# Kernel optimization log

Measured on AMD Instinct MI355X. Metric: run time of the kernel, lower is better.

Reference implementation:

```python
import jax, jax.numpy as jnp
import numpy as np

K, S, PAD = 3, 2, 1
C, HID = 16, 128
H, W = 256, 256
EPS = 1e-6


def _unfold(xp, k, s):
    # xp: (B, C, Hp, Wp) -> (B, C*k*k, L), torch.nn.Unfold ordering (c major, then kh, kw)
    B, Cc, Hp, Wp = xp.shape
    Ho = (Hp - k) // s + 1
    Wo = (Wp - k) // s + 1
    cols = jnp.stack(
        [xp[:, :, i:i + (Ho - 1) * s + 1:s, j:j + (Wo - 1) * s + 1:s]
         for i in range(k) for j in range(k)], axis=2)  # (B, C, k*k, Ho, Wo)
    return cols.reshape(B, Cc * k * k, Ho * Wo), Ho, Wo


def _fold(patches, Hp, Wp, Ho, Wo, k, s):
    # patches: (B, C*k*k, L) -> scatter-add into (B, C, Hp, Wp)
    B = patches.shape[0]
    p = patches.reshape(B, -1, k, k, Ho, Wo)
    out = jnp.zeros((B, p.shape[1], Hp, Wp), dtype=patches.dtype)
    for i in range(k):
        for j in range(k):
            out = out.at[:, :, i:i + (Ho - 1) * s + 1:s, j:j + (Wo - 1) * s + 1:s].add(p[:, :, i, j])
    return out


def setup_inputs() -> dict:
    key = jax.random.key(0)
    ks = jax.random.split(key, 7)
    P = C * K * K  # 144
    x = jax.random.normal(ks[0], (32, C, H, W), dtype=jnp.float32)
    W1 = jax.random.normal(ks[1], (P, HID), dtype=jnp.float32) * (1.0 / np.sqrt(P))
    b1 = jax.random.normal(ks[2], (HID,), dtype=jnp.float32) * 0.01
    W2 = jax.random.normal(ks[3], (HID, P), dtype=jnp.float32) * (1.0 / np.sqrt(HID))
    b2 = jax.random.normal(ks[4], (P,), dtype=jnp.float32) * 0.01
    Wc = jax.random.normal(ks[5], (C, C), dtype=jnp.float32) * (1.0 / np.sqrt(C))
    bc = jax.random.normal(ks[6], (C,), dtype=jnp.float32) * 0.01
    return {"x": x, "W1": W1, "b1": b1, "W2": W2, "b2": b2, "Wc": Wc, "bc": bc}


def reference(x, W1, b1, W2, b2, Wc, bc):
    Hp, Wp = H + 2 * PAD, W + 2 * PAD
    xp = jnp.pad(x, ((0, 0), (0, 0), (PAD, PAD), (PAD, PAD)), mode='reflect')
    patches, Ho, Wo = _unfold(xp, K, S)          # (B, P, L)
    t = patches.transpose(0, 2, 1)               # (B, L, P)
    hcat = jax.nn.relu(t @ W1 + b1)              # (B, L, HID)
    out_p = (hcat @ W2 + b2).transpose(0, 2, 1)  # (B, P, L)
    folded = _fold(out_p, Hp, Wp, Ho, Wo, K, S)
    counts = _fold(jnp.ones_like(out_p), Hp, Wp, Ho, Wo, K, S)
    normalized = folded / (counts + EPS)
    logits = jnp.einsum('oc,bchw->bohw', Wc, normalized) + bc[None, :, None, None]
    attn = jax.nn.softmax(logits, axis=1)        # Softmax2d = softmax over channels
    modulated = normalized * attn
    return modulated[:, :, PAD:PAD + H, PAD:PAD + W]
```

## Files before the change

kernel.cpp:

```cpp
#include <hip/hip_runtime.h>
#include <math.h>

#define CC   16
#define HH   256
#define WW   256
#define HIDN 128
#define PDIM 144
#define K1PAD 160
#define PITCH_H 136

typedef _Float16 half8 __attribute__((ext_vector_type(8)));
typedef float   f32x4 __attribute__((ext_vector_type(4)));

#define MFMA16(a, b, c) __builtin_amdgcn_mfma_f32_16x16x32_f16((a), (b), (c), 0, 0, 0)

#define O_BYTES   ((size_t)524288 * 144 * 2)
#define W1T_OFF   O_BYTES
#define W1T_BYTES ((size_t)128 * K1PAD * 2)
#define W2T_OFF   (W1T_OFF + W1T_BYTES)
#define W2T_BYTES ((size_t)144 * 128 * 2)
#define WS_NEEDED (W2T_OFF + W2T_BYTES)

__device__ __forceinline__ void load_lds16(const float* g, float* l)
{
#if __has_builtin(__builtin_amdgcn_global_load_lds)
    __builtin_amdgcn_global_load_lds(
        (const __attribute__((address_space(1))) unsigned int*)g,
        (__attribute__((address_space(3))) unsigned int*)l, 16, 0, 0);
#else
    *(float4*)l = *(const float4*)g;
#endif
}

__device__ __forceinline__ void load_lds16h(const _Float16* g, _Float16* l)
{
#if __has_builtin(__builtin_amdgcn_global_load_lds)
    __builtin_amdgcn_global_load_lds(
        (const __attribute__((address_space(1))) unsigned int*)g,
        (__attribute__((address_space(3))) unsigned int*)l, 16, 0, 0);
#else
    *(float4*)(void*)l = *(const float4*)(const void*)g;
#endif
}

__global__ __launch_bounds__(256) void prep_kernel(
    const float* __restrict__ W1, const float* __restrict__ W2,
    _Float16* __restrict__ W1T, _Float16* __restrict__ W2T)
{
    const int idx = blockIdx.x * 256 + threadIdx.x;
    if (idx < 128 * K1PAD) {
        const int n = idx / K1PAD;
        const int k = idx - n * K1PAD;
        const int tap = k >> 4;
        const int c   = k & 15;
        W1T[idx] = (tap < 9) ? (_Float16)W1[(c * 9 + tap) * HIDN + n] : (_Float16)0.f;
    }
    if (idx < 144 * 128) {
        const int nn = idx >> 7;
        const int k  = idx & 127;
        const int tap = nn >> 4;
        const int c   = nn & 15;
        W2T[nn * 128 + k] = (_Float16)W2[k * PDIM + (c * 9 + tap)];
    }
}

__global__ __launch_bounds__(256) void mlp_kernel(
    const float* __restrict__ x,
    const _Float16* __restrict__ W1T, const float* __restrict__ b1,
    const _Float16* __restrict__ W2T, const float* __restrict__ b2,
    _Float16* __restrict__ og)
{
    __shared__ __align__(16) char smem[73728];
    _Float16* xT    = (_Float16*)smem;
    float*    xrowF = (float*)(smem + 24576);
    _Float16* hT    = (_Float16*)(smem + 24576);

    const int tid   = threadIdx.x;
    const int a     = blockIdx.x & 127;
    const int batch = blockIdx.x >> 7;
    const float* xb = x + (size_t)batch * CC * HH * WW;

    #pragma unroll
    for (int it = 0; it < 12; ++it) {
        const int idx = tid + it * 256;
        const int i   = idx >> 10;
        const int c   = (idx >> 6) & 15;
        const int q   = idx & 63;
        int ym = 2 * a + i - 1;
        if (ym < 0) ym = 1;
        load_lds16(xb + ((c * HH + ym) * WW + 4 * q), xrowF + idx * 4);
    }
    __syncthreads();

    #pragma unroll
    for (int k = 0; k < 3; ++k) {
        const int u  = tid + k * 256;
        const int i  = u >> 8;
        const int xm = u & 255;
        const float* rbase = xrowF + i * 4096 + xm;
        half8 lo, hi;
        #pragma unroll
        for (int c = 0; c < 8; ++c) lo[c] = (_Float16)rbase[c * 256];
        #pragma unroll
        for (int c = 0; c < 8; ++c) hi[c] = (_Float16)rbase[(c + 8) * 256];
        int s = u << 4;
        s ^= (s & 0x1C0) >> 3;
        *(half8*)(xT + s)       = lo;
        *(half8*)(xT + (s ^ 8)) = hi;
    }
    __syncthreads();

    const int wid  = tid >> 6;
    const int lane = tid & 63;
    const int l15  = lane & 15;
    const int quad = lane >> 4;
    const int qh   = quad >> 1;
    const int c0   = (quad & 1) * 8;

    {
        half8 bfr0[5], bfr1[5];
        float bias0, bias1;
        {
            const int nt0 = 2 * wid, nt1 = 2 * wid + 1;
            const _Float16* w0 = W1T + (nt0 * 16 + l15) * K1PAD + quad * 8;
            const _Float16* w1 = W1T + (nt1 * 16 + l15) * K1PAD + quad * 8;
            #pragma unroll
            for (int ks = 0; ks < 5; ++ks) {
                bfr0[ks] = *(const half8*)(w0 + ks * 32);
                bfr1[ks] = *(const half8*)(w1 + ks * 32);
            }
            bias0 = b1[nt0 * 16 + l15];
            bias1 = b1[nt1 * 16 + l15];
        }
        int koffU[5], koffF[5];
        #pragma unroll
        for (int ks = 0; ks < 5; ++ks) {
            int tap = 2 * ks + qh;
            if (tap > 8) tap = 8;
            const int i   = (tap * 11) >> 5;
            const int j   = tap - 3 * i;
            const int xmU = 2 * l15 + j - 1;
            const int xmF = (xmU < 0) ? 1 : xmU;
            koffU[ks] = (i << 12) + (xmU << 4) + c0;
            koffF[ks] = (i << 12) + (xmF << 4) + c0;
        }

        #define G1_STEP(MT, KO)                                                   \
        {                                                                         \
            f32x4 acc0 = {0.f, 0.f, 0.f, 0.f};                                    \
            f32x4 acc1 = {0.f, 0.f, 0.f, 0.f};                                    \
            _Pragma("unroll")                                                     \
            for (int ks = 0; ks < 5; ++ks) {                                      \
                int ix = KO[ks] + ((MT) << 9);                                    \
                ix ^= (ix & 0x1C0) >> 3;                                          \
                const half8 af = *(const half8*)(xT + ix);                        \
                acc0 = MFMA16(af, bfr0[ks], acc0);                                \
                acc1 = MFMA16(af, bfr1[ks], acc1);                                \
            }                                                                     \
            _Pragma("unroll")                                                     \
            for (int r = 0; r < 4; ++r) {                                         \
                const int row = (MT) * 16 + quad * 4 + r;                         \
                float h0 = acc0[r] + bias0;                                       \
                float h1 = acc1[r] + bias1;                                       \
                hT[row * PITCH_H + (2 * wid) * 16 + l15]     = (_Float16)(h0 > 0.f ? h0 : 0.f); \
                hT[row * PITCH_H + (2 * wid + 1) * 16 + l15] = (_Float16)(h1 > 0.f ? h1 : 0.f); \
            }                                                                     \
        }

        G1_STEP(0, koffF)
        for (int mt = 1; mt < 8; ++mt) G1_STEP(mt, koffU)
        #undef G1_STEP
    }
    __syncthreads();

    const size_t abase = ((size_t)batch * 128 + a) * 9;
    {
        half8 bfr2[2][4];
        float bias2[2];
        #pragma unroll
        for (int n = 0; n < 2; ++n) {
            const int nt = wid + n * 4;
            const _Float16* w2row = W2T + (nt * 16 + l15) * 128 + quad * 8;
            #pragma unroll
            for (int ks = 0; ks < 4; ++ks)
                bfr2[n][ks] = *(const half8*)(w2row + ks * 32);
            bias2[n] = b2[l15 * 9 + nt];
        }
        _Float16* ognA = og + (abase + wid) * 2048;
        _Float16* ognB = og + (abase + wid + 4) * 2048;
        for (int mt = 0; mt < 8; ++mt) {
            f32x4 acc0 = {0.f, 0.f, 0.f, 0.f};
            f32x4 acc1 = {0.f, 0.f, 0.f, 0.f};
            const _Float16* arow = hT + (mt * 16 + l15) * PITCH_H + quad * 8;
            #pragma unroll
            for (int ks = 0; ks < 4; ++ks) {
                const half8 af = *(const half8*)(arow + ks * 32);
                acc0 = MFMA16(af, bfr2[0][ks], acc0);
                acc1 = MFMA16(af, bfr2[1][ks], acc1);
            }
            #pragma unroll
            for (int r = 0; r < 4; ++r) {
                const int b = mt * 16 + quad * 4 + r;
                ognA[b * 16 + l15] = (_Float16)(acc0[r] + bias2[0]);
                ognB[b * 16 + l15] = (_Float16)(acc1[r] + bias2[1]);
            }
        }
        {
            half8 bfr8[4];
            const _Float16* w2row = W2T + (8 * 16 + l15) * 128 + quad * 8;
            #pragma unroll
            for (int ks = 0; ks < 4; ++ks)
                bfr8[ks] = *(const half8*)(w2row + ks * 32);
            const float bias8 = b2[l15 * 9 + 8];
            _Float16* ogn = og + (abase + 8) * 2048;
            #pragma unroll
            for (int m = 0; m < 2; ++m) {
                const int mt = 2 * wid + m;
                f32x4 acc = {0.f, 0.f, 0.f, 0.f};
                const _Float16* arow = hT + (mt * 16 + l15) * PITCH_H + quad * 8;
                #pragma unroll
                for (int ks = 0; ks < 4; ++ks)
                    acc = MFMA16(*(const half8*)(arow + ks * 32), bfr8[ks], acc);
                #pragma unroll
                for (int r = 0; r < 4; ++r) {
                    const int b = mt * 16 + quad * 4 + r;
                    ogn[b * 16 + l15] = (_Float16)(acc[r] + bias8);
                }
            }
        }
    }
}

__global__ __launch_bounds__(256) void gather_kernel(
    const _Float16* __restrict__ og, const float* __restrict__ Wc,
    const float* __restrict__ bc, float* __restrict__ out)
{
    __shared__ __align__(16) _Float16 sPl[9 * 2048];
    __shared__ float sWc[256];
    __shared__ float sbc[16];

    const int tid   = threadIdx.x;
    const int a     = blockIdx.x & 127;
    const int batch = blockIdx.x >> 7;

    sWc[tid] = Wc[tid];
    if (tid < 16) sbc[tid] = bc[tid];

    const size_t pb = (size_t)batch * 128;
    const int a1 = (a < 127) ? a + 1 : 127;
    const int srcOff = (tid ^ ((tid >> 3) & 7)) * 8;
    #pragma unroll
    for (int p = 0; p < 9; ++p) {
        const int ap  = (p < 6) ? a : a1;
        const int tap = (p < 3) ? (3 + p) : ((p < 6) ? (3 + p) : (p - 6));
        const _Float16* src = og + ((pb + ap) * 9 + tap) * 2048 + srcOff;
        load_lds16h(src, sPl + p * 2048 + tid * 8);
    }
    __syncthreads();

    const int x = tid;
    int blist[2], jlist[2], nb = 0;
    if ((x + 1) & 1) { blist[0] = x >> 1; jlist[0] = 1; nb = 1; }
    else {
        if (x < 255) { blist[nb] = (x + 1) >> 1; jlist[nb] = 0; ++nb; }
        blist[nb] = (x - 1) >> 1; jlist[nb] = 2; ++nb;
    }
    const int na1 = (a < 127) ? 2 : 1;

    float nrm0[CC], nrm1[CC];
    #pragma unroll
    for (int c = 0; c < CC; ++c) { nrm0[c] = 0.f; nrm1[c] = 0.f; }

    #define ACC_PLANE(P, B, DST)                                             \
    {                                                                        \
        int s = (B) * 16;                                                    \
        s ^= (s & 0x1C0) >> 3;                                               \
        const _Float16* orow = sPl + (P) * 2048;                             \
        const half8 o0 = *(const half8*)(orow + s);                          \
        const half8 o1 = *(const half8*)(orow + (s ^ 8));                    \
        _Pragma("unroll")                                                    \
        for (int e = 0; e < 8; ++e) { DST[e] += (float)o0[e]; DST[8 + e] += (float)o1[e]; } \
    }

    for (int v = 0; v < 2; ++v) {
        if (v >= nb) break;
        const int j = jlist[v];
        const int b = blist[v];
        ACC_PLANE(j,     b, nrm0)
        ACC_PLANE(3 + j, b, nrm1)
        if (na1 == 2) ACC_PLANE(6 + j, b, nrm1)
    }
    #undef ACC_PLANE

    const float inv0 = 1.f / ((float)nb + 1e-6f);
    const float inv1 = 1.f / ((float)(na1 * nb) + 1e-6f);
    #pragma unroll
    for (int c = 0; c < CC; ++c) { nrm0[c] *= inv0; nrm1[c] *= inv1; }

    const size_t obase = ((size_t)batch * CC) * (HH * WW) + (size_t)(2 * a) * WW + x;
    #pragma unroll
    for (int rowsel = 0; rowsel < 2; ++rowsel) {
        const float* nrm = rowsel ? nrm1 : nrm0;
        float lg[CC];
        #pragma unroll
        for (int o = 0; o < CC; ++o) {
            float s = sbc[o];
            #pragma unroll
            for (int c = 0; c < CC; ++c) s = fmaf(sWc[o * CC + c], nrm[c], s);
            lg[o] = s;
        }
        float mx = lg[0];
        #pragma unroll
        for (int o = 1; o < CC; ++o) mx = fmaxf(mx, lg[o]);
        float se = 0.f;
        #pragma unroll
        for (int o = 0; o < CC; ++o) { lg[o] = expf(lg[o] - mx); se += lg[o]; }
        const float isum = 1.f / se;
        const size_t ob = obase + (size_t)rowsel * WW;
        #pragma unroll
        for (int c = 0; c < CC; ++c)
            out[ob + (size_t)c * (HH * WW)] = nrm[c] * lg[c] * isum;
    }
}

#define HT_PITCH 68
__global__ __launch_bounds__(256) void mlp_fold_kernel_fb(
    const float* __restrict__ x,  const float* __restrict__ W1,
    const float* __restrict__ b1, const float* __restrict__ W2,
    const float* __restrict__ b2, float* __restrict__ folded)
{
    __shared__ __align__(16) float pT[PDIM * 64];
    __shared__ __align__(16) float hT[HIDN * HT_PITCH];
    const int tid = threadIdx.x;
    const int tile = blockIdx.x & 255;
    const int b = blockIdx.x >> 8;
    const int tile_base = tile * 64;
    const float* xb = x + (size_t)b * CC * HH * WW;
    for (int idx = tid; idx < PDIM * 64; idx += 256) {
        const int p = idx >> 6, lo = idx & 63;
        const int c = p / 9, rem = p - c * 9, i = rem / 3, j = rem - i * 3;
        const int l = tile_base + lo, a = l >> 7, bb = l & 127;
        int ym = 2 * a + i - 1, xm = 2 * bb + j - 1;
        if (ym < 0) ym = 1;
        if (xm < 0) xm = 1;
        pT[p * 64 + lo] = xb[(c * HH + ym) * WW + xm];
    }
    __syncthreads();
    {
        const int cg = tid & 31, rg = tid >> 5, rbase = rg * 8;
        float acc[8][4];
        #pragma unroll
        for (int m = 0; m < 8; ++m)
            #pragma unroll
            for (int jj = 0; jj < 4; ++jj) acc[m][jj] = 0.f;
        for (int k = 0; k < PDIM; ++k) {
            const float4 w = *reinterpret_cast<const float4*>(W1 + k * HIDN + cg * 4);
            const float4 pa = *reinterpret_cast<const float4*>(pT + k * 64 + rbase);
            const float4 pb2 = *reinterpret_cast<const float4*>(pT + k * 64 + rbase + 4);
            const float pv[8] = {pa.x, pa.y, pa.z, pa.w, pb2.x, pb2.y, pb2.z, pb2.w};
            const float wv[4] = {w.x, w.y, w.z, w.w};
            #pragma unroll
            for (int m = 0; m < 8; ++m)
                #pragma unroll
                for (int jj = 0; jj < 4; ++jj) acc[m][jj] = fmaf(pv[m], wv[jj], acc[m][jj]);
        }
        #pragma unroll
        for (int jj = 0; jj < 4; ++jj) {
            const int jcol = cg * 4 + jj;
            const float bj = b1[jcol];
            #pragma unroll
            for (int m = 0; m < 8; ++m) {
                const float hval = acc[m][jj] + bj;
                hT[jcol * HT_PITCH + rbase + m] = hval > 0.f ? hval : 0.f;
            }
        }
    }
    __syncthreads();
    {
        const int cg2 = tid & 15, rg2 = tid >> 4, rb2 = rg2 * 4;
        float acc2[4][9];
        #pragma unroll
        for (int m = 0; m < 4; ++m)
            #pragma unroll
            for (int jj = 0; jj < 9; ++jj) acc2[m][jj] = 0.f;
        const float* w2base = W2 + cg2 * 9;
        for (int h = 0; h < HIDN; ++h) {
            const float4 hv4 = *reinterpret_cast<const float4*>(hT + h * HT_PITCH + rb2);
            const float hv[4] = {hv4.x, hv4.y, hv4.z, hv4.w};
            float wv[9];
            #pragma unroll
            for (int jj = 0; jj < 9; ++jj) wv[jj] = w2base[h * PDIM + jj];
            #pragma unroll
            for (int m = 0; m < 4; ++m)
                #pragma unroll
                for (int jj = 0; jj < 9; ++jj) acc2[m][jj] = fmaf(hv[m], wv[jj], acc2[m][jj]);
        }
        float bv[9];
        #pragma unroll
        for (int jj = 0; jj < 9; ++jj) bv[jj] = b2[cg2 * 9 + jj];
        float* fb = folded + ((size_t)b * CC + cg2) * (HH * WW);
        #pragma unroll
        for (int m = 0; m < 4; ++m) {
            const int l = tile_base + rb2 + m, a = l >> 7, bb = l & 127;
            #pragma unroll
            for (int jj = 0; jj < 9; ++jj) {
                const int i = jj / 3, j2 = jj - i * 3;
                const int ypad = 2 * a + i, xpad = 2 * bb + j2;
                if (ypad >= 1 && xpad >= 1)
                    atomicAdd(fb + (ypad - 1) * WW + (xpad - 1), acc2[m][jj] + bv[jj]);
            }
        }
    }
}

__global__ __launch_bounds__(256) void norm_softmax_kernel_fb(
    float* __restrict__ out, const float* __restrict__ Wc, const float* __restrict__ bc)
{
    const int xo = threadIdx.x, yo = blockIdx.x & 255, b = blockIdx.x >> 8;
    const int yp = yo + 1, xp = xo + 1;
    const float cy = ((yp & 1) || yp == 256) ? 1.f : 2.f;
    const float cx = ((xp & 1) || xp == 256) ? 1.f : 2.f;
    const float inv = 1.f / (cy * cx + 1e-6f);
    const size_t base = ((size_t)b * CC) * (HH * WW) + (size_t)yo * WW + xo;
    float nrm[CC];
    #pragma unroll
    for (int c = 0; c < CC; ++c) nrm[c] = out[base + (size_t)c * (HH * WW)] * inv;
    float logits[CC];
    #pragma unroll
    for (int o = 0; o < CC; ++o) {
        float s = bc[o];
        #pragma unroll
        for (int c = 0; c < CC; ++c) s = fmaf(Wc[o * CC + c], nrm[c], s);
        logits[o] = s;
    }
    float mx = logits[0];
    #pragma unroll
    for (int o = 1; o < CC; ++o) mx = fmaxf(mx, logits[o]);
    float se = 0.f;
    #pragma unroll
    for (int o = 0; o < CC; ++o) { logits[o] = expf(logits[o] - mx); se += logits[o]; }
    const float isum = 1.f / se;
    #pragma unroll
    for (int c = 0; c < CC; ++c)
        out[base + (size_t)c * (HH * WW)] = nrm[c] * logits[c] * isum;
}

extern "C" void kernel_launch(void* const* d_in, const int* in_sizes, int n_in,
                              void* d_out, int out_size, void* d_ws, size_t ws_size,
                              hipStream_t stream)
{
    const float* x  = (const float*)d_in[0];
    const float* W1 = (const float*)d_in[1];
    const float* b1 = (const float*)d_in[2];
    const float* W2 = (const float*)d_in[3];
    const float* b2 = (const float*)d_in[4];
    const float* Wc = (const float*)d_in[5];
    const float* bc = (const float*)d_in[6];
    float* out = (float*)d_out;

    if (ws_size >= WS_NEEDED) {
        _Float16* og  = (_Float16*)d_ws;
        _Float16* W1T = (_Float16*)((char*)d_ws + W1T_OFF);
        _Float16* W2T = (_Float16*)((char*)d_ws + W2T_OFF);

        prep_kernel<<<dim3(80), dim3(256), 0, stream>>>(W1, W2, W1T, W2T);
        mlp_kernel<<<dim3(32 * 128), dim3(256), 0, stream>>>(x, W1T, b1, W2T, b2, og);
        gather_kernel<<<dim3(32 * 128), dim3(256), 0, stream>>>(og, Wc, bc, out);
    } else {
        hipMemsetAsync(d_out, 0, (size_t)out_size * sizeof(float), stream);
        mlp_fold_kernel_fb<<<dim3(32 * 256), dim3(256), 0, stream>>>(x, W1, b1, W2, b2, out);
        norm_softmax_kernel_fb<<<dim3(32 * 256), dim3(256), 0, stream>>>(out, Wc, bc);
    }
}
```

Measured before the change: 332.2 us.

## Split MLP blocks into column halves with halo and double gather threads per block

The MLP kernel now gives each block half an output row (128 columns), with a one-column halo loaded separately. This cuts LDS per block from 72KB to about 37KB and adds a launch bound of 4 blocks per CU, doubling the grid. The gather kernel uses 512 threads so each thread handles one output row instead of two, which lowers register pressure and spreads the softmax work. The cost is extra halo handling, some redundant loads of x, and more blocks to launch.

```diff
diff --git a/kernel.cpp b/kernel.cpp
--- a/kernel.cpp
+++ b/kernel.cpp
@@ -8,6 +8,8 @@
 #define PDIM 144
 #define K1PAD 160
 #define PITCH_H 136
+#define XT_PITCH 2080
+#define XT_HALFS 6272
 
 typedef _Float16 half8 __attribute__((ext_vector_type(8)));
 typedef float   f32x4 __attribute__((ext_vector_type(4)));
@@ -64,49 +66,65 @@
     }
 }
 
-__global__ __launch_bounds__(256) void mlp_kernel(
+__global__ __launch_bounds__(256, 4) void mlp_kernel(
     const float* __restrict__ x,
     const _Float16* __restrict__ W1T, const float* __restrict__ b1,
     const _Float16* __restrict__ W2T, const float* __restrict__ b2,
     _Float16* __restrict__ og)
 {
-    __shared__ __align__(16) char smem[73728];
+    __shared__ __align__(16) char smem[12544 + 24576];
     _Float16* xT    = (_Float16*)smem;
-    float*    xrowF = (float*)(smem + 24576);
-    _Float16* hT    = (_Float16*)(smem + 24576);
+    float*    xrowF = (float*)(smem + 12544);
+    _Float16* hT    = (_Float16*)(smem + 12544);
 
     const int tid   = threadIdx.x;
-    const int a     = blockIdx.x & 127;
-    const int batch = blockIdx.x >> 7;
+    const int h     = blockIdx.x & 1;
+    const int a     = (blockIdx.x >> 1) & 127;
+    const int batch = blockIdx.x >> 8;
     const float* xb = x + (size_t)batch * CC * HH * WW;
 
-    #pragma unroll
-    for (int it = 0; it < 12; ++it) {
-        const int idx = tid + it * 256;
-        const int i   = idx >> 10;
-        const int c   = (idx >> 6) & 15;
-        const int q   = idx & 63;
+    float halo = 0.f;
+    if (h && tid < 48) {
+        const int i = tid >> 4, c = tid & 15;
         int ym = 2 * a + i - 1;
         if (ym < 0) ym = 1;
-        load_lds16(xb + ((c * HH + ym) * WW + 4 * q), xrowF + idx * 4);
+        halo = xb[(c * HH + ym) * WW + 127];
+    }
+
+    #pragma unroll
+    for (int it = 0; it < 6; ++it) {
+        const int idx = tid + it * 256;
+        const int i   = idx >> 9;
+        const int c   = (idx >> 5) & 15;
+        const int q   = idx & 31;
+        int ym = 2 * a + i - 1;
+        if (ym < 0) ym = 1;
+        load_lds16(xb + ((c * HH + ym) * WW + h * 128 + 4 * q), xrowF + idx * 4);
     }
     __syncthreads();
 
     #pragma unroll
-    for (int k = 0; k < 3; ++k) {
-        const int u  = tid + k * 256;
-        const int i  = u >> 8;
-        const int xm = u & 255;
-        const float* rbase = xrowF + i * 4096 + xm;
-        half8 lo, hi;
-        #pragma unroll
-        for (int c = 0; c < 8; ++c) lo[c] = (_Float16)rbase[c * 256];
-        #pragma unroll
-        for (int c = 0; c < 8; ++c) hi[c] = (_Float16)rbase[(c + 8) * 256];
-        int s = u << 4;
+    for (int k = 0; k < 2; ++k) {
+        const int u = tid + k * 256;
+        if (u < 384) {
+            const int i  = u >> 7;
+            const int xm = u & 127;
+            const float* rbase = xrowF + i * 2048 + xm;
+            half8 lo, hi;
+            #pragma unroll
+            for (int c = 0; c < 8; ++c) lo[c] = (_Float16)rbase[c * 128];
+            #pragma unroll
+            for (int c = 0; c < 8; ++c) hi[c] = (_Float16)rbase[(c + 8) * 128];
+            int s = i * XT_PITCH + (xm + 1) * 16;
+            s ^= (s & 0x1C0) >> 3;
+            *(half8*)(xT + s)       = lo;
+            *(half8*)(xT + (s ^ 8)) = hi;
+        }
+    }
+    if (h && tid < 48) {
+        int s = (tid >> 4) * XT_PITCH + (tid & 15);
         s ^= (s & 0x1C0) >> 3;
-        *(half8*)(xT + s)       = lo;
-        *(half8*)(xT + (s ^ 8)) = hi;
+        xT[s] = (_Float16)halo;
     }
     __syncthreads();
 
@@ -137,12 +155,12 @@
         for (int ks = 0; ks < 5; ++ks) {
             int tap = 2 * ks + qh;
             if (tap > 8) tap = 8;
-            const int i   = (tap * 11) >> 5;
-            const int j   = tap - 3 * i;
-            const int xmU = 2 * l15 + j - 1;
-            const int xmF = (xmU < 0) ? 1 : xmU;
-            koffU[ks] = (i << 12) + (xmU << 4) + c0;
-            koffF[ks] = (i << 12) + (xmF << 4) + c0;
+            const int i = (tap * 11) >> 5;
+            const int j = tap - 3 * i;
+            const int slotU = 2 * l15 + j;
+            const int slotF = (h == 0 && slotU == 0) ? 2 : slotU;
+            koffU[ks] = i * XT_PITCH + slotU * 16 + c0;
+            koffF[ks] = i * XT_PITCH + slotF * 16 + c0;
         }
 
         #define G1_STEP(MT, KO)                                                   \
@@ -168,12 +186,14 @@
         }
 
         G1_STEP(0, koffF)
-        for (int mt = 1; mt < 8; ++mt) G1_STEP(mt, koffU)
+        #pragma unroll
+        for (int mt = 1; mt < 4; ++mt) G1_STEP(mt, koffU)
         #undef G1_STEP
     }
     __syncthreads();
 
     const size_t abase = ((size_t)batch * 128 + a) * 9;
+    const int hoff = h * 1024;
     {
         half8 bfr2[2][4];
         float bias2[2];
@@ -186,9 +206,10 @@
                 bfr2[n][ks] = *(const half8*)(w2row + ks * 32);
             bias2[n] = b2[l15 * 9 + nt];
         }
-        _Float16* ognA = og + (abase + wid) * 2048;
-        _Float16* ognB = og + (abase + wid + 4) * 2048;
-        for (int mt = 0; mt < 8; ++mt) {
+        _Float16* ognA = og + (abase + wid) * 2048 + hoff;
+        _Float16* ognB = og + (abase + wid + 4) * 2048 + hoff;
+        #pragma unroll
+        for (int mt = 0; mt < 4; ++mt) {
             f32x4 acc0 = {0.f, 0.f, 0.f, 0.f};
             f32x4 acc1 = {0.f, 0.f, 0.f, 0.f};
             const _Float16* arow = hT + (mt * 16 + l15) * PITCH_H + quad * 8;
@@ -212,26 +233,23 @@
             for (int ks = 0; ks < 4; ++ks)
                 bfr8[ks] = *(const half8*)(w2row + ks * 32);
             const float bias8 = b2[l15 * 9 + 8];
-            _Float16* ogn = og + (abase + 8) * 2048;
-            #pragma unroll
-            for (int m = 0; m < 2; ++m) {
-                const int mt = 2 * wid + m;
-                f32x4 acc = {0.f, 0.f, 0.f, 0.f};
-                const _Float16* arow = hT + (mt * 16 + l15) * PITCH_H + quad * 8;
-                #pragma unroll
-                for (int ks = 0; ks < 4; ++ks)
-                    acc = MFMA16(*(const half8*)(arow + ks * 32), bfr8[ks], acc);
-                #pragma unroll
-                for (int r = 0; r < 4; ++r) {
-                    const int b = mt * 16 + quad * 4 + r;
-                    ogn[b * 16 + l15] = (_Float16)(acc[r] + bias8);
-                }
-            }
-        }
-    }
-}
-
-__global__ __launch_bounds__(256) void gather_kernel(
+            _Float16* ogn = og + (abase + 8) * 2048 + hoff;
+            const int mt = wid;
+            f32x4 acc = {0.f, 0.f, 0.f, 0.f};
+            const _Float16* arow = hT + (mt * 16 + l15) * PITCH_H + quad * 8;
+            #pragma unroll
+            for (int ks = 0; ks < 4; ++ks)
+                acc = MFMA16(*(const half8*)(arow + ks * 32), bfr8[ks], acc);
+            #pragma unroll
+            for (int r = 0; r < 4; ++r) {
+                const int b = mt * 16 + quad * 4 + r;
+                ogn[b * 16 + l15] = (_Float16)(acc[r] + bias8);
+            }
+        }
+    }
+}
+
+__global__ __launch_bounds__(512) void gather_kernel(
     const _Float16* __restrict__ og, const float* __restrict__ Wc,
     const float* __restrict__ bc, float* __restrict__ out)
 {
@@ -243,35 +261,42 @@
     const int a     = blockIdx.x & 127;
     const int batch = blockIdx.x >> 7;
 
-    sWc[tid] = Wc[tid];
-    if (tid < 16) sbc[tid] = bc[tid];
-
     const size_t pb = (size_t)batch * 128;
     const int a1 = (a < 127) ? a + 1 : 127;
-    const int srcOff = (tid ^ ((tid >> 3) & 7)) * 8;
-    #pragma unroll
-    for (int p = 0; p < 9; ++p) {
-        const int ap  = (p < 6) ? a : a1;
-        const int tap = (p < 3) ? (3 + p) : ((p < 6) ? (3 + p) : (p - 6));
-        const _Float16* src = og + ((pb + ap) * 9 + tap) * 2048 + srcOff;
-        load_lds16h(src, sPl + p * 2048 + tid * 8);
-    }
-    __syncthreads();
-
-    const int x = tid;
+
+    #pragma unroll
+    for (int it = 0; it < 5; ++it) {
+        const int idx = tid + it * 512;
+        if (idx < 2304) {
+            const int p      = idx >> 8;
+            const int ch     = idx & 255;
+            const int src_ch = ch ^ ((ch >> 3) & 7);
+            const int ap  = (p < 6) ? a : a1;
+            const int tap = (p < 6) ? (3 + p) : (p - 6);
+            const _Float16* src = og + ((pb + ap) * 9 + tap) * 2048 + src_ch * 8;
+            load_lds16h(src, sPl + p * 2048 + ch * 8);
+        }
+    }
+    if (tid < 256) sWc[tid] = Wc[tid];
+    if (tid < 16)  sbc[tid] = bc[tid];
+
+    const int x      = tid & 255;
+    const int rowsel = tid >> 8;
     int blist[2], jlist[2], nb = 0;
-    if ((x + 1) & 1) { blist[0] = x >> 1; jlist[0] = 1; nb = 1; }
+    if ((x + 1) & 1) { blist[0] = x >> 1; jlist[0] = 1; nb = 1; blist[1] = blist[0]; jlist[1] = jlist[0]; }
     else {
         if (x < 255) { blist[nb] = (x + 1) >> 1; jlist[nb] = 0; ++nb; }
         blist[nb] = (x - 1) >> 1; jlist[nb] = 2; ++nb;
+        if (nb == 1) { blist[1] = blist[0]; jlist[1] = jlist[0]; }
     }
     const int na1 = (a < 127) ? 2 : 1;
-
-    float nrm0[CC], nrm1[CC];
-    #pragma unroll
-    for (int c = 0; c < CC; ++c) { nrm0[c] = 0.f; nrm1[c] = 0.f; }
-
-    #define ACC_PLANE(P, B, DST)                                             \
+    __syncthreads();
+
+    float nrm[CC];
+    #pragma unroll
+    for (int c = 0; c < CC; ++c) nrm[c] = 0.f;
+
+    #define ACC_PLANE(P, B)                                                  \
     {                                                                        \
         int s = (B) * 16;                                                    \
         s ^= (s & 0x1C0) >> 3;                                               \
@@ -279,48 +304,50 @@
         const half8 o0 = *(const half8*)(orow + s);                          \
         const half8 o1 = *(const half8*)(orow + (s ^ 8));                    \
         _Pragma("unroll")                                                    \
-        for (int e = 0; e < 8; ++e) { DST[e] += (float)o0[e]; DST[8 + e] += (float)o1[e]; } \
-    }
-
+        for (int e = 0; e < 8; ++e) { nrm[e] += (float)o0[e]; nrm[8 + e] += (float)o1[e]; } \
+    }
+
+    #pragma unroll
     for (int v = 0; v < 2; ++v) {
-        if (v >= nb) break;
-        const int j = jlist[v];
-        const int b = blist[v];
-        ACC_PLANE(j,     b, nrm0)
-        ACC_PLANE(3 + j, b, nrm1)
-        if (na1 == 2) ACC_PLANE(6 + j, b, nrm1)
+        if (v < nb) {
+            const int j = jlist[v];
+            const int b = blist[v];
+            if (rowsel == 0) {
+                ACC_PLANE(j, b)
+            } else {
+                ACC_PLANE(3 + j, b)
+                if (na1 == 2) ACC_PLANE(6 + j, b)
+            }
+        }
     }
     #undef ACC_PLANE
 
-    const float inv0 = 1.f / ((float)nb + 1e-6f);
-    const float inv1 = 1.f / ((float)(na1 * nb) + 1e-6f);
-    #pragma unroll
-    for (int c = 0; c < CC; ++c) { nrm0[c] *= inv0; nrm1[c] *= inv1; }
-
-    const size_t obase = ((size_t)batch * CC) * (HH * WW) + (size_t)(2 * a) * WW + x;
-    #pragma unroll
-    for (int rowsel = 0; rowsel < 2; ++rowsel) {
-        const float* nrm = rowsel ? nrm1 : nrm0;
-        float lg[CC];
-        #pragma unroll
-        for (int o = 0; o < CC; ++o) {
-            float s = sbc[o];
-            #pragma unroll
-            for (int c = 0; c < CC; ++c) s = fmaf(sWc[o * CC + c], nrm[c], s);
-            lg[o] = s;
-        }
-        float mx = lg[0];
-        #pragma unroll
-        for (int o = 1; o < CC; ++o) mx = fmaxf(mx, lg[o]);
-        float se = 0.f;
-        #pragma unroll
-        for (int o = 0; o < CC; ++o) { lg[o] = expf(lg[o] - mx); se += lg[o]; }
-        const float isum = 1.f / se;
-        const size_t ob = obase + (size_t)rowsel * WW;
-        #pragma unroll
-        for (int c = 0; c < CC; ++c)
-            out[ob + (size_t)c * (HH * WW)] = nrm[c] * lg[c] * isum;
-    }
+    const float cnt = rowsel ? (float)(na1 * nb) : (float)nb;
+    const float inv = 1.f / (cnt + 1e-6f);
+    #pragma unroll
+    for (int c = 0; c < CC; ++c) nrm[c] *= inv;
+
+    float lg[CC];
+    #pragma unroll
+    for (int o = 0; o < CC; ++o) {
+        float s = sbc[o];
+        #pragma unroll
+        for (int c = 0; c < CC; ++c) s = fmaf(sWc[o * CC + c], nrm[c], s);
+        lg[o] = s;
+    }
+    float mx = lg[0];
+    #pragma unroll
+    for (int o = 1; o < CC; ++o) mx = fmaxf(mx, lg[o]);
+    float se = 0.f;
+    #pragma unroll
+    for (int o = 0; o < CC; ++o) { lg[o] = expf(lg[o] - mx); se += lg[o]; }
+    const float isum = 1.f / se;
+
+    const size_t ob = ((size_t)batch * CC) * (HH * WW)
+                    + (size_t)(2 * a + rowsel) * WW + x;
+    #pragma unroll
+    for (int c = 0; c < CC; ++c)
+        out[ob + (size_t)c * (HH * WW)] = nrm[c] * lg[c] * isum;
 }
 
 #define HT_PITCH 68
@@ -464,8 +491,8 @@
         _Float16* W2T = (_Float16*)((char*)d_ws + W2T_OFF);
 
         prep_kernel<<<dim3(80), dim3(256), 0, stream>>>(W1, W2, W1T, W2T);
-        mlp_kernel<<<dim3(32 * 128), dim3(256), 0, stream>>>(x, W1T, b1, W2T, b2, og);
-        gather_kernel<<<dim3(32 * 128), dim3(256), 0, stream>>>(og, Wc, bc, out);
+        mlp_kernel<<<dim3(32 * 256), dim3(256), 0, stream>>>(x, W1T, b1, W2T, b2, og);
+        gather_kernel<<<dim3(32 * 128), dim3(512), 0, stream>>>(og, Wc, bc, out);
     } else {
         hipMemsetAsync(d_out, 0, (size_t)out_size * sizeof(float), stream);
         mlp_fold_kernel_fb<<<dim3(32 * 256), dim3(256), 0, stream>>>(x, W1, b1, W2, b2, out);
```

After: 365.2 us. 9.9% more time.

## Fuse MLP and fold/softmax gather into one kernel with recomputed neighbor row

Applied to the files above, without the earlier changes.

Merges the MLP kernel and the gather/normalize/softmax kernel into a single fused kernel, so the fp16 patch-output intermediate no longer goes through global memory. Each block computes its own patch row's six taps into LDS, writes the even output row, then recomputes the MLP for the next patch row to get the three taps needed for the odd output row. This removes about 150MB of intermediate write/read traffic and one launch. In exchange the MLP is partly recomputed (about 1.5x GEMM work), and each block runs more serialized phases with extra barriers.

```diff
diff --git a/kernel.cpp b/kernel.cpp
--- a/kernel.cpp
+++ b/kernel.cpp
@@ -14,8 +14,7 @@
 
 #define MFMA16(a, b, c) __builtin_amdgcn_mfma_f32_16x16x32_f16((a), (b), (c), 0, 0, 0)
 
-#define O_BYTES   ((size_t)524288 * 144 * 2)
-#define W1T_OFF   O_BYTES
+#define W1T_OFF   0
 #define W1T_BYTES ((size_t)128 * K1PAD * 2)
 #define W2T_OFF   (W1T_OFF + W1T_BYTES)
 #define W2T_BYTES ((size_t)144 * 128 * 2)
@@ -32,17 +31,6 @@
 #endif
 }
 
-__device__ __forceinline__ void load_lds16h(const _Float16* g, _Float16* l)
-{
-#if __has_builtin(__builtin_amdgcn_global_load_lds)
-    __builtin_amdgcn_global_load_lds(
-        (const __attribute__((address_space(1))) unsigned int*)g,
-        (__attribute__((address_space(3))) unsigned int*)l, 16, 0, 0);
-#else
-    *(float4*)(void*)l = *(const float4*)(const void*)g;
-#endif
-}
-
 __global__ __launch_bounds__(256) void prep_kernel(
     const float* __restrict__ W1, const float* __restrict__ W2,
     _Float16* __restrict__ W1T, _Float16* __restrict__ W2T)
@@ -64,34 +52,24 @@
     }
 }
 
-__global__ __launch_bounds__(256) void mlp_kernel(
-    const float* __restrict__ x,
-    const _Float16* __restrict__ W1T, const float* __restrict__ b1,
-    const _Float16* __restrict__ W2T, const float* __restrict__ b2,
-    _Float16* __restrict__ og)
-{
-    __shared__ __align__(16) char smem[73728];
-    _Float16* xT    = (_Float16*)smem;
-    float*    xrowF = (float*)(smem + 24576);
-    _Float16* hT    = (_Float16*)(smem + 24576);
-
-    const int tid   = threadIdx.x;
-    const int a     = blockIdx.x & 127;
-    const int batch = blockIdx.x >> 7;
-    const float* xb = x + (size_t)batch * CC * HH * WW;
-
+
+__device__ __forceinline__ void stage_rows(const float* __restrict__ xb,
+                                           float* xrowF, int arow, int tid)
+{
     #pragma unroll
     for (int it = 0; it < 12; ++it) {
         const int idx = tid + it * 256;
         const int i   = idx >> 10;
         const int c   = (idx >> 6) & 15;
         const int q   = idx & 63;
-        int ym = 2 * a + i - 1;
+        int ym = 2 * arow + i - 1;
         if (ym < 0) ym = 1;
         load_lds16(xb + ((c * HH + ym) * WW + 4 * q), xrowF + idx * 4);
     }
-    __syncthreads();
-
+}
+
+__device__ __forceinline__ void transpose_x(const float* xrowF, _Float16* xT, int tid)
+{
     #pragma unroll
     for (int k = 0; k < 3; ++k) {
         const int u  = tid + k * 256;
@@ -108,7 +86,191 @@
         *(half8*)(xT + s)       = lo;
         *(half8*)(xT + (s ^ 8)) = hi;
     }
-    __syncthreads();
+}
+
+__device__ __forceinline__ void gemm1(const _Float16* xT, _Float16* hT,
+                                      const _Float16* __restrict__ W1T,
+                                      const float* __restrict__ b1,
+                                      int wid, int l15, int quad, int qh, int c0)
+{
+    half8 bfr0[5], bfr1[5];
+    float bias0, bias1;
+    {
+        const int nt0 = 2 * wid, nt1 = 2 * wid + 1;
+        const _Float16* w0 = W1T + (nt0 * 16 + l15) * K1PAD + quad * 8;
+        const _Float16* w1 = W1T + (nt1 * 16 + l15) * K1PAD + quad * 8;
+        #pragma unroll
+        for (int ks = 0; ks < 5; ++ks) {
+            bfr0[ks] = *(const half8*)(w0 + ks * 32);
+            bfr1[ks] = *(const half8*)(w1 + ks * 32);
+        }
+        bias0 = b1[nt0 * 16 + l15];
+        bias1 = b1[nt1 * 16 + l15];
+    }
+    int koffU[5], koffF[5];
+    #pragma unroll
+    for (int ks = 0; ks < 5; ++ks) {
+        int tap = 2 * ks + qh;
+        if (tap > 8) tap = 8;
+        const int i   = (tap * 11) >> 5;
+        const int j   = tap - 3 * i;
+        const int xmU = 2 * l15 + j - 1;
+        const int xmF = (xmU < 0) ? 1 : xmU;
+        koffU[ks] = (i << 12) + (xmU << 4) + c0;
+        koffF[ks] = (i << 12) + (xmF << 4) + c0;
+    }
+    #define G1_STEP(MT, KO)                                                   \
+    {                                                                         \
+        f32x4 acc0 = {0.f, 0.f, 0.f, 0.f};                                    \
+        f32x4 acc1 = {0.f, 0.f, 0.f, 0.f};                                    \
+        _Pragma("unroll")                                                     \
+        for (int ks = 0; ks < 5; ++ks) {                                      \
+            int ix = KO[ks] + ((MT) << 9);                                    \
+            ix ^= (ix & 0x1C0) >> 3;                                          \
+            const half8 af = *(const half8*)(xT + ix);                        \
+            acc0 = MFMA16(af, bfr0[ks], acc0);                                \
+            acc1 = MFMA16(af, bfr1[ks], acc1);                                \
+        }                                                                     \
+        _Pragma("unroll")                                                     \
+        for (int r = 0; r < 4; ++r) {                                         \
+            const int row = (MT) * 16 + quad * 4 + r;                         \
+            float h0 = acc0[r] + bias0;                                       \
+            float h1 = acc1[r] + bias1;                                       \
+            hT[row * PITCH_H + (2 * wid) * 16 + l15]     = (_Float16)(h0 > 0.f ? h0 : 0.f); \
+            hT[row * PITCH_H + (2 * wid + 1) * 16 + l15] = (_Float16)(h1 > 0.f ? h1 : 0.f); \
+        }                                                                     \
+    }
+    G1_STEP(0, koffF)
+    for (int mt = 1; mt < 8; ++mt) G1_STEP(mt, koffU)
+    #undef G1_STEP
+}
+
+__device__ __forceinline__ void gemm2_six(const _Float16* hT, _Float16* sPl,
+                                          const _Float16* __restrict__ W2T,
+                                          const float* __restrict__ b2,
+                                          int wid, int l15, int quad)
+{
+    const int wm = wid >> 1;
+    const int wn = wid & 1;
+    half8 bfr[3][4];
+    float bias[3];
+    #pragma unroll
+    for (int t = 0; t < 3; ++t) {
+        const int tap = 3 + wn * 3 + t;
+        const _Float16* w2row = W2T + (tap * 16 + l15) * 128 + quad * 8;
+        #pragma unroll
+        for (int ks = 0; ks < 4; ++ks)
+            bfr[t][ks] = *(const half8*)(w2row + ks * 32);
+        bias[t] = b2[l15 * 9 + tap];
+    }
+    #pragma unroll
+    for (int m = 0; m < 4; ++m) {
+        const int mt = wm * 4 + m;
+        const _Float16* arow = hT + (mt * 16 + l15) * PITCH_H + quad * 8;
+        half8 af[4];
+        #pragma unroll
+        for (int ks = 0; ks < 4; ++ks) af[ks] = *(const half8*)(arow + ks * 32);
+        #pragma unroll
+        for (int t = 0; t < 3; ++t) {
+            f32x4 acc = {0.f, 0.f, 0.f, 0.f};
+            #pragma unroll
+            for (int ks = 0; ks < 4; ++ks) acc = MFMA16(af[ks], bfr[t][ks], acc);
+            const int p = wn * 3 + t;
+            #pragma unroll
+            for (int r = 0; r < 4; ++r) {
+                const int bcol = mt * 16 + quad * 4 + r;
+                int sw = bcol * 16 + l15;
+                sw ^= (sw & 0x1C0) >> 3;
+                sPl[p * 2048 + sw] = (_Float16)(acc[r] + bias[t]);
+            }
+        }
+    }
+}
+
+__device__ __forceinline__ void gemm2_three(const _Float16* hT, _Float16* sPl,
+                                            const _Float16* __restrict__ W2T,
+                                            const float* __restrict__ b2,
+                                            int wid, int l15, int quad)
+{
+    half8 bfr[3][4];
+    float bias[3];
+    #pragma unroll
+    for (int t = 0; t < 3; ++t) {
+        const _Float16* w2row = W2T + (t * 16 + l15) * 128 + quad * 8;
+        #pragma unroll
+        for (int ks = 0; ks < 4; ++ks)
+            bfr[t][ks] = *(const half8*)(w2row + ks * 32);
+        bias[t] = b2[l15 * 9 + t];
+    }
+    #pragma unroll
+    for (int m = 0; m < 2; ++m) {
+        const int mt = 2 * wid + m;
+        const _Float16* arow = hT + (mt * 16 + l15) * PITCH_H + quad * 8;
+        half8 af[4];
+        #pragma unroll
+        for (int ks = 0; ks < 4; ++ks) af[ks] = *(const half8*)(arow + ks * 32);
+        #pragma unroll
+        for (int t = 0; t < 3; ++t) {
+            f32x4 acc = {0.f, 0.f, 0.f, 0.f};
+            #pragma unroll
+            for (int ks = 0; ks < 4; ++ks) acc = MFMA16(af[ks], bfr[t][ks], acc);
+            #pragma unroll
+            for (int r = 0; r < 4; ++r) {
+                const int bcol = mt * 16 + quad * 4 + r;
+                int sw = bcol * 16 + l15;
+                sw ^= (sw & 0x1C0) >> 3;
+                sPl[t * 2048 + sw] = (_Float16)(acc[r] + bias[t]);
+            }
+        }
+    }
+}
+
+__device__ __forceinline__ void mix_softmax_store(const float* nrm,
+                                                  const float* sWc, const float* sbc,
+                                                  float* outp)
+{
+    float lg[CC];
+    #pragma unroll
+    for (int o = 0; o < CC; ++o) {
+        float s = sbc[o];
+        #pragma unroll
+        for (int c = 0; c < CC; ++c) s = fmaf(sWc[o * CC + c], nrm[c], s);
+        lg[o] = s;
+    }
+    float mx = lg[0];
+    #pragma unroll
+    for (int o = 1; o < CC; ++o) mx = fmaxf(mx, lg[o]);
+    float se = 0.f;
+    #pragma unroll
+    for (int o = 0; o < CC; ++o) { lg[o] = expf(lg[o] - mx); se += lg[o]; }
+    const float isum = 1.f / se;
+    #pragma unroll
+    for (int c = 0; c < CC; ++c)
+        outp[(size_t)c * (HH * WW)] = nrm[c] * lg[c] * isum;
+}
+
+__global__ __launch_bounds__(256) void fused_kernel(
+    const float* __restrict__ x,
+    const _Float16* __restrict__ W1T, const float* __restrict__ b1,
+    const _Float16* __restrict__ W2T, const float* __restrict__ b2,
+    const float* __restrict__ Wc, const float* __restrict__ bc,
+    float* __restrict__ out)
+{
+    __shared__ __align__(16) char smem[73728];
+    _Float16* xT    = (_Float16*)smem;
+    _Float16* sPl   = (_Float16*)smem;
+    _Float16* hT    = (_Float16*)(smem + 24576);
+    float*    xrowF = (float*)(smem + 24576);
+    __shared__ float sWc[256];
+    __shared__ float sbc[16];
+
+    const int tid   = threadIdx.x;
+    const int a     = blockIdx.x & 127;
+    const int batch = blockIdx.x >> 7;
+    const float* xb = x + (size_t)batch * CC * HH * WW;
+
+    sWc[tid] = Wc[tid];
+    if (tid < 16) sbc[tid] = bc[tid];
 
     const int wid  = tid >> 6;
     const int lane = tid & 63;
@@ -117,155 +279,25 @@
     const int qh   = quad >> 1;
     const int c0   = (quad & 1) * 8;
 
-    {
-        half8 bfr0[5], bfr1[5];
-        float bias0, bias1;
-        {
-            const int nt0 = 2 * wid, nt1 = 2 * wid + 1;
-            const _Float16* w0 = W1T + (nt0 * 16 + l15) * K1PAD + quad * 8;
-            const _Float16* w1 = W1T + (nt1 * 16 + l15) * K1PAD + quad * 8;
-            #pragma unroll
-            for (int ks = 0; ks < 5; ++ks) {
-                bfr0[ks] = *(const half8*)(w0 + ks * 32);
-                bfr1[ks] = *(const half8*)(w1 + ks * 32);
-            }
-            bias0 = b1[nt0 * 16 + l15];
-            bias1 = b1[nt1 * 16 + l15];
-        }
-        int koffU[5], koffF[5];
-        #pragma unroll
-        for (int ks = 0; ks < 5; ++ks) {
-            int tap = 2 * ks + qh;
-            if (tap > 8) tap = 8;
-            const int i   = (tap * 11) >> 5;
-            const int j   = tap - 3 * i;
-            const int xmU = 2 * l15 + j - 1;
-            const int xmF = (xmU < 0) ? 1 : xmU;
-            koffU[ks] = (i << 12) + (xmU << 4) + c0;
-            koffF[ks] = (i << 12) + (xmF << 4) + c0;
-        }
-
-        #define G1_STEP(MT, KO)                                                   \
-        {                                                                         \
-            f32x4 acc0 = {0.f, 0.f, 0.f, 0.f};                                    \
-            f32x4 acc1 = {0.f, 0.f, 0.f, 0.f};                                    \
-            _Pragma("unroll")                                                     \
-            for (int ks = 0; ks < 5; ++ks) {                                      \
-                int ix = KO[ks] + ((MT) << 9);                                    \
-                ix ^= (ix & 0x1C0) >> 3;                                          \
-                const half8 af = *(const half8*)(xT + ix);                        \
-                acc0 = MFMA16(af, bfr0[ks], acc0);                                \
-                acc1 = MFMA16(af, bfr1[ks], acc1);                                \
-            }                                                                     \
-            _Pragma("unroll")                                                     \
-            for (int r = 0; r < 4; ++r) {                                         \
-                const int row = (MT) * 16 + quad * 4 + r;                         \
-                float h0 = acc0[r] + bias0;                                       \
-                float h1 = acc1[r] + bias1;                                       \
-                hT[row * PITCH_H + (2 * wid) * 16 + l15]     = (_Float16)(h0 > 0.f ? h0 : 0.f); \
-                hT[row * PITCH_H + (2 * wid + 1) * 16 + l15] = (_Float16)(h1 > 0.f ? h1 : 0.f); \
-            }                                                                     \
-        }
-
-        G1_STEP(0, koffF)
-        for (int mt = 1; mt < 8; ++mt) G1_STEP(mt, koffU)
-        #undef G1_STEP
-    }
-    __syncthreads();
-
-    const size_t abase = ((size_t)batch * 128 + a) * 9;
-    {
-        half8 bfr2[2][4];
-        float bias2[2];
-        #pragma unroll
-        for (int n = 0; n < 2; ++n) {
-            const int nt = wid + n * 4;
-            const _Float16* w2row = W2T + (nt * 16 + l15) * 128 + quad * 8;
-            #pragma unroll
-            for (int ks = 0; ks < 4; ++ks)
-                bfr2[n][ks] = *(const half8*)(w2row + ks * 32);
-            bias2[n] = b2[l15 * 9 + nt];
-        }
-        _Float16* ognA = og + (abase + wid) * 2048;
-        _Float16* ognB = og + (abase + wid + 4) * 2048;
-        for (int mt = 0; mt < 8; ++mt) {
-            f32x4 acc0 = {0.f, 0.f, 0.f, 0.f};
-            f32x4 acc1 = {0.f, 0.f, 0.f, 0.f};
-            const _Float16* arow = hT + (mt * 16 + l15) * PITCH_H + quad * 8;
-            #pragma unroll
-            for (int ks = 0; ks < 4; ++ks) {
-                const half8 af = *(const half8*)(arow + ks * 32);
-                acc0 = MFMA16(af, bfr2[0][ks], acc0);
-                acc1 = MFMA16(af, bfr2[1][ks], acc1);
-            }
-            #pragma unroll
-            for (int r = 0; r < 4; ++r) {
-                const int b = mt * 16 + quad * 4 + r;
-                ognA[b * 16 + l15] = (_Float16)(acc0[r] + bias2[0]);
-                ognB[b * 16 + l15] = (_Float16)(acc1[r] + bias2[1]);
-            }
-        }
-        {
-            half8 bfr8[4];
-            const _Float16* w2row = W2T + (8 * 16 + l15) * 128 + quad * 8;
-            #pragma unroll
-            for (int ks = 0; ks < 4; ++ks)
-                bfr8[ks] = *(const half8*)(w2row + ks * 32);
-            const float bias8 = b2[l15 * 9 + 8];
-            _Float16* ogn = og + (abase + 8) * 2048;
-            #pragma unroll
-            for (int m = 0; m < 2; ++m) {
-                const int mt = 2 * wid + m;
-                f32x4 acc = {0.f, 0.f, 0.f, 0.f};
-                const _Float16* arow = hT + (mt * 16 + l15) * PITCH_H + quad * 8;
-                #pragma unroll
-                for (int ks = 0; ks < 4; ++ks)
-                    acc = MFMA16(*(const half8*)(arow + ks * 32), bfr8[ks], acc);
-                #pragma unroll
-                for (int r = 0; r < 4; ++r) {
-                    const int b = mt * 16 + quad * 4 + r;
-                    ogn[b * 16 + l15] = (_Float16)(acc[r] + bias8);
-                }
-            }
-        }
-    }
-}
-
-__global__ __launch_bounds__(256) void gather_kernel(
-    const _Float16* __restrict__ og, const float* __restrict__ Wc,
-    const float* __restrict__ bc, float* __restrict__ out)
-{
-    __shared__ __align__(16) _Float16 sPl[9 * 2048];
-    __shared__ float sWc[256];
-    __shared__ float sbc[16];
-
-    const int tid   = threadIdx.x;
-    const int a     = blockIdx.x & 127;
-    const int batch = blockIdx.x >> 7;
-
-    sWc[tid] = Wc[tid];
-    if (tid < 16) sbc[tid] = bc[tid];
-
-    const size_t pb = (size_t)batch * 128;
-    const int a1 = (a < 127) ? a + 1 : 127;
-    const int srcOff = (tid ^ ((tid >> 3) & 7)) * 8;
-    #pragma unroll
-    for (int p = 0; p < 9; ++p) {
-        const int ap  = (p < 6) ? a : a1;
-        const int tap = (p < 3) ? (3 + p) : ((p < 6) ? (3 + p) : (p - 6));
-        const _Float16* src = og + ((pb + ap) * 9 + tap) * 2048 + srcOff;
-        load_lds16h(src, sPl + p * 2048 + tid * 8);
-    }
-    __syncthreads();
-
-    const int x = tid;
+    stage_rows(xb, xrowF, a, tid);
+    __syncthreads();
+    transpose_x(xrowF, xT, tid);
+    __syncthreads();
+    gemm1(xT, hT, W1T, b1, wid, l15, quad, qh, c0);
+    __syncthreads();
+    gemm2_six(hT, sPl, W2T, b2, wid, l15, quad);
+    __syncthreads();
+
+    if (a < 127) stage_rows(xb, xrowF, a + 1, tid);
+
+    const int xo = tid;
     int blist[2], jlist[2], nb = 0;
-    if ((x + 1) & 1) { blist[0] = x >> 1; jlist[0] = 1; nb = 1; }
+    if ((xo + 1) & 1) { blist[0] = xo >> 1; jlist[0] = 1; nb = 1; blist[1] = blist[0]; jlist[1] = jlist[0]; }
     else {
-        if (x < 255) { blist[nb] = (x + 1) >> 1; jlist[nb] = 0; ++nb; }
-        blist[nb] = (x - 1) >> 1; jlist[nb] = 2; ++nb;
-    }
-    const int na1 = (a < 127) ? 2 : 1;
+        if (xo < 255) { blist[nb] = (xo + 1) >> 1; jlist[nb] = 0; ++nb; }
+        blist[nb] = (xo - 1) >> 1; jlist[nb] = 2; ++nb;
+        if (nb == 1) { blist[1] = blist[0]; jlist[1] = jlist[0]; }
+    }
 
     float nrm0[CC], nrm1[CC];
     #pragma unroll
@@ -282,44 +314,45 @@
         for (int e = 0; e < 8; ++e) { DST[e] += (float)o0[e]; DST[8 + e] += (float)o1[e]; } \
     }
 
+    #pragma unroll
     for (int v = 0; v < 2; ++v) {
-        if (v >= nb) break;
-        const int j = jlist[v];
-        const int b = blist[v];
-        ACC_PLANE(j,     b, nrm0)
-        ACC_PLANE(3 + j, b, nrm1)
-        if (na1 == 2) ACC_PLANE(6 + j, b, nrm1)
+        if (v < nb) {
+            ACC_PLANE(jlist[v],     blist[v], nrm0)
+            ACC_PLANE(3 + jlist[v], blist[v], nrm1)
+        }
+    }
+
+    {
+        const float inv0 = 1.f / ((float)nb + 1e-6f);
+        float nrmE[CC];
+        #pragma unroll
+        for (int c = 0; c < CC; ++c) nrmE[c] = nrm0[c] * inv0;
+        float* outp = out + ((size_t)batch * CC) * (HH * WW) + (size_t)(2 * a) * WW + xo;
+        mix_softmax_store(nrmE, sWc, sbc, outp);
+    }
+    __syncthreads();
+
+    if (a < 127) {
+        transpose_x(xrowF, xT, tid);
+        __syncthreads();
+        gemm1(xT, hT, W1T, b1, wid, l15, quad, qh, c0);
+        __syncthreads();
+        gemm2_three(hT, sPl, W2T, b2, wid, l15, quad);
+        __syncthreads();
+        #pragma unroll
+        for (int v = 0; v < 2; ++v) {
+            if (v < nb) ACC_PLANE(jlist[v], blist[v], nrm1)
+        }
     }
     #undef ACC_PLANE
 
-    const float inv0 = 1.f / ((float)nb + 1e-6f);
-    const float inv1 = 1.f / ((float)(na1 * nb) + 1e-6f);
-    #pragma unroll
-    for (int c = 0; c < CC; ++c) { nrm0[c] *= inv0; nrm1[c] *= inv1; }
-
-    const size_t obase = ((size_t)batch * CC) * (HH * WW) + (size_t)(2 * a) * WW + x;
-    #pragma unroll
-    for (int rowsel = 0; rowsel < 2; ++rowsel) {
-        const float* nrm = rowsel ? nrm1 : nrm0;
-        float lg[CC];
-        #pragma unroll
-        for (int o = 0; o < CC; ++o) {
-            float s = sbc[o];
-            #pragma unroll
-            for (int c = 0; c < CC; ++c) s = fmaf(sWc[o * CC + c], nrm[c], s);
-            lg[o] = s;
-        }
-        float mx = lg[0];
-        #pragma unroll
-        for (int o = 1; o < CC; ++o) mx = fmaxf(mx, lg[o]);
-        float se = 0.f;
-        #pragma unroll
-        for (int o = 0; o < CC; ++o) { lg[o] = expf(lg[o] - mx); se += lg[o]; }
-        const float isum = 1.f / se;
-        const size_t ob = obase + (size_t)rowsel * WW;
-        #pragma unroll
-        for (int c = 0; c < CC; ++c)
-            out[ob + (size_t)c * (HH * WW)] = nrm[c] * lg[c] * isum;
+    {
+        const int na1 = (a < 127) ? 2 : 1;
+        const float inv1 = 1.f / ((float)(na1 * nb) + 1e-6f);
+        #pragma unroll
+        for (int c = 0; c < CC; ++c) nrm1[c] *= inv1;
+        float* outp = out + ((size_t)batch * CC) * (HH * WW) + (size_t)(2 * a + 1) * WW + xo;
+        mix_softmax_store(nrm1, sWc, sbc, outp);
     }
 }
 
@@ -459,13 +492,12 @@
     float* out = (float*)d_out;
 
     if (ws_size >= WS_NEEDED) {
-        _Float16* og  = (_Float16*)d_ws;
         _Float16* W1T = (_Float16*)((char*)d_ws + W1T_OFF);
         _Float16* W2T = (_Float16*)((char*)d_ws + W2T_OFF);
 
         prep_kernel<<<dim3(80), dim3(256), 0, stream>>>(W1, W2, W1T, W2T);
-        mlp_kernel<<<dim3(32 * 128), dim3(256), 0, stream>>>(x, W1T, b1, W2T, b2, og);
-        gather_kernel<<<dim3(32 * 128), dim3(256), 0, stream>>>(og, Wc, bc, out);
+        fused_kernel<<<dim3(32 * 128), dim3(256), 0, stream>>>(
+            x, W1T, b1, W2T, b2, Wc, bc, out);
     } else {
         hipMemsetAsync(d_out, 0, (size_t)out_size * sizeof(float), stream);
         mlp_fold_kernel_fb<<<dim3(32 * 256), dim3(256), 0, stream>>>(x, W1, b1, W2, b2, out);
```

Result: slower. 357.2 us (+7.5%).
